# Performance work log

Measured on AMD Instinct MI355X. Metric: run time of the kernel, lower is better.

## Reference

```python
import jax, jax.numpy as jnp
import numpy as np

B, T, C = 256, 2048, 64
WINDOW_RATIO = 0.1
SCALES = (0.5, 2.0)
WARP_SIZE = int(np.ceil(WINDOW_RATIO * T))            # 205, matches np.ceil(...).astype(int)
L_MAX = (T - WARP_SIZE) + int(WARP_SIZE * max(SCALES))  # max warped length (scale=2.0) = 2253


def setup_inputs() -> dict:
    key = jax.random.key(0)
    k1, k2, k3 = jax.random.split(key, 3)
    x = jax.random.normal(k1, (B, T, C), dtype=jnp.float32)
    # np.random.choice(scales, B)
    warp_scales = jnp.asarray(SCALES, jnp.float32)[jax.random.randint(k2, (B,), 0, len(SCALES))]
    # np.random.randint(low=1, high=T - warp_size - 1, size=B)
    window_starts = jax.random.randint(k3, (B,), 1, T - WARP_SIZE - 1).astype(jnp.int32)
    return {"x": x, "warp_scales": warp_scales, "window_starts": window_starts}


def _lerp_gather(arr, pos, max_idx):
    # arr: [B, L, C]; pos: [B, N] fractional indices -> [B, N, C] linear interp
    p0 = jnp.floor(pos)
    frac = (pos - p0)[..., None]
    i0 = p0.astype(jnp.int32)
    i1 = jnp.minimum(i0 + 1, max_idx)
    g0 = jnp.take_along_axis(arr, i0[..., None], axis=1)
    g1 = jnp.take_along_axis(arr, i1[..., None], axis=1)
    return g0 * (1.0 - frac) + g1 * frac


def _window_warp(x, warp_scales, window_starts):
    Bx, Tx, Cx = x.shape
    # int(warp_size * scale): truncation == floor for positive values
    new_len = jnp.floor(WARP_SIZE * warp_scales)          # [B] float, resampled window length
    L = (Tx - WARP_SIZE) + new_len                        # [B] float, total warped length per sample
    start = window_starts.astype(x.dtype)[:, None]        # [B,1]
    nl = new_len[:, None]                                 # [B,1]

    # Stage 1: build warped sequence of padded length L_MAX via fractional gather from x.
    # warped[j] = x[j]                       for j < start
    #           = interp(x window) at s_win  for start <= j < start+new_len
    #           = x[j - new_len + warp_size] for j >= start+new_len (garbage past L, never read)
    j = jnp.arange(L_MAX, dtype=x.dtype)[None, :]         # [1, L_MAX]
    in_win = (j >= start) & (j < start + nl)
    after = j >= start + nl
    s_win = start + (j - start) * (WARP_SIZE - 1) / jnp.maximum(nl - 1.0, 1.0)
    s = jnp.where(in_win, s_win, jnp.where(after, j - nl + WARP_SIZE, j))
    s = jnp.clip(s, 0.0, Tx - 1)
    warped = _lerp_gather(x, s, Tx - 1)                   # [B, L_MAX, C]

    # Stage 2: np.interp(arange(T), linspace(0, T-1, L), warped) == linear interp of
    # warped at fractional index u = t * (L-1) / (T-1)
    t = jnp.arange(Tx, dtype=x.dtype)[None, :]            # [1, T]
    u = t * (L[:, None] - 1.0) / (Tx - 1.0)
    u = jnp.clip(u, 0.0, L[:, None] - 1.0)
    return _lerp_gather(warped, u, L_MAX - 1)             # [B, T, C]


def reference(x, warp_scales, window_starts):
    return _window_warp(x, warp_scales, window_starts)
```

## Files before the change

kernel.cpp:

```cpp
#include <hip/hip_runtime.h>

constexpr int Bn     = 256;
constexpr int Tn     = 2048;
constexpr int Cn     = 64;
constexpr int WARPSZ = 205;
constexpr int LMAX   = 2253;

typedef float f32x4 __attribute__((ext_vector_type(4)));

__device__ __forceinline__ void map_j(float jf, float start, float nl, float rdenom,
                                      int& i0, int& i1, float& fr) {
    bool in_win = (jf >= start) && (jf < start + nl);
    bool after  = (jf >= start + nl);
    float s_win   = start + (jf - start) * rdenom;
    float s_after = jf - nl + (float)WARPSZ;
    float s = in_win ? s_win : (after ? s_after : jf);
    s = fminf(fmaxf(s, 0.0f), (float)(Tn - 1));
    float p0 = floorf(s);
    fr = s - p0;
    i0 = (int)p0;
    i1 = min(i0 + 1, Tn - 1);
}

__global__ __launch_bounds__(256) void window_warp_kernel(
        const float* __restrict__ x,
        const float* __restrict__ scales,
        const int*   __restrict__ starts,
        float*       __restrict__ out) {
    int b     = blockIdx.x >> 6;
    int tbase = ((blockIdx.x & 63) << 5) | (threadIdx.x >> 4);
    int cg    = threadIdx.x & 15;

    float scale = scales[b];
    float start = (float)starts[b];
    float nl    = floorf((float)WARPSZ * scale);
    float Lm1   = (float)(Tn - WARPSZ) + nl - 1.0f;
    float rdenom = (float)(WARPSZ - 1) / fmaxf(nl - 1.0f, 1.0f);

    const f32x4* __restrict__ xb   = (const f32x4*)(x   + (size_t)b * (Tn * Cn));
    f32x4*       __restrict__ outb = (f32x4*)      (out + (size_t)b * (Tn * Cn));

    int   i00[2], i01[2], i10[2], i11[2];
    float f0[2], f1[2], fu[2];

    #pragma unroll
    for (int k = 0; k < 2; ++k) {
        int t = tbase + 16 * k;
        float u = ((float)t * Lm1) / (float)(Tn - 1);
        u = fminf(fmaxf(u, 0.0f), Lm1);
        float q0 = floorf(u);
        fu[k] = u - q0;
        int j0 = (int)q0;
        int j1 = min(j0 + 1, LMAX - 1);
        map_j((float)j0, start, nl, rdenom, i00[k], i01[k], f0[k]);
        map_j((float)j1, start, nl, rdenom, i10[k], i11[k], f1[k]);
    }

    f32x4 A0[2], A1[2], B0[2], B1[2];
    #pragma unroll
    for (int k = 0; k < 2; ++k) {
        A0[k] = xb[i00[k] * 16 + cg];
        A1[k] = xb[i01[k] * 16 + cg];
        B0[k] = xb[i10[k] * 16 + cg];
        B1[k] = xb[i11[k] * 16 + cg];
    }

    #pragma unroll
    for (int k = 0; k < 2; ++k) {
        int t = tbase + 16 * k;
        float g0 = 1.0f - f0[k], g1 = 1.0f - f1[k], gu = 1.0f - fu[k];
        f32x4 v0 = A0[k] * g0 + A1[k] * f0[k];
        f32x4 v1 = B0[k] * g1 + B1[k] * f1[k];
        f32x4 r  = v0 * gu + v1 * fu[k];
        __builtin_nontemporal_store(r, &outb[t * 16 + cg]);
    }
}

extern "C" void kernel_launch(void* const* d_in, const int* in_sizes, int n_in,
                              void* d_out, int out_size, void* d_ws, size_t ws_size,
                              hipStream_t stream) {
    const float* x      = (const float*)d_in[0];
    const float* scales = (const float*)d_in[1];
    const int*   starts = (const int*)d_in[2];
    float* out = (float*)d_out;

    int total_threads = Bn * Tn * (Cn / 4) / 2;
    int blocks = total_threads / 256;
    window_warp_kernel<<<blocks, 256, 0, stream>>>(x, scales, starts, out);
}
```

Measured before the change: 228.1 us.

## Stage per-block input rows in LDS via async global_load_lds and remap block order

```diff
diff --git a/kernel.cpp b/kernel.cpp
--- a/kernel.cpp
+++ b/kernel.cpp
@@ -1,10 +1,14 @@
 #include <hip/hip_runtime.h>
+#include <stdint.h>
 
 constexpr int Bn     = 256;
 constexpr int Tn     = 2048;
 constexpr int Cn     = 64;
 constexpr int WARPSZ = 205;
 constexpr int LMAX   = 2253;
+
+constexpr int TB = 32;
+constexpr int NR = 72;
 
 typedef float f32x4 __attribute__((ext_vector_type(4)));
 
@@ -27,8 +31,13 @@
         const float* __restrict__ scales,
         const int*   __restrict__ starts,
         float*       __restrict__ out) {
-    int b     = blockIdx.x >> 6;
-    int tbase = ((blockIdx.x & 63) << 5) | (threadIdx.x >> 4);
+    __shared__ f32x4 smem[NR * (Cn / 4)];
+
+    int n    = blockIdx.x;
+    int bidx = ((n & 7) << 11) | (n >> 3);
+    int b     = bidx >> 6;
+    int t0    = (bidx & 63) << 5;
+    int tslot = threadIdx.x >> 4;
     int cg    = threadIdx.x & 15;
 
     float scale = scales[b];
@@ -37,15 +46,33 @@
     float Lm1   = (float)(Tn - WARPSZ) + nl - 1.0f;
     float rdenom = (float)(WARPSZ - 1) / fmaxf(nl - 1.0f, 1.0f);
 
-    const f32x4* __restrict__ xb   = (const f32x4*)(x   + (size_t)b * (Tn * Cn));
-    f32x4*       __restrict__ outb = (f32x4*)      (out + (size_t)b * (Tn * Cn));
+    float u0 = ((float)t0 * Lm1) / (float)(Tn - 1);
+    u0 = fminf(fmaxf(u0, 0.0f), Lm1);
+    int j00 = (int)floorf(u0);
+    int r0a, r0b; float fr0;
+    map_j((float)j00, start, nl, rdenom, r0a, r0b, fr0);
+    int rbase = min(r0a, Tn - NR);
+
+    {
+        const float* gbase = x + (size_t)b * (Tn * Cn) + rbase * Cn;
+        int wave = threadIdx.x >> 6;
+        int lane = threadIdx.x & 63;
+        float* sm = (float*)smem;
+        #pragma unroll
+        for (int c = wave; c < (NR * Cn * 4) / 1024; c += 4) {
+            __builtin_amdgcn_global_load_lds(
+                (const __attribute__((address_space(1))) uint32_t*)(gbase + c * 256 + lane * 4),
+                (__attribute__((address_space(3))) uint32_t*)(sm + c * 256),
+                16, 0, 0);
+        }
+    }
+    __syncthreads();
 
     int   i00[2], i01[2], i10[2], i11[2];
     float f0[2], f1[2], fu[2];
-
     #pragma unroll
     for (int k = 0; k < 2; ++k) {
-        int t = tbase + 16 * k;
+        int t = t0 + tslot + 16 * k;
         float u = ((float)t * Lm1) / (float)(Tn - 1);
         u = fminf(fmaxf(u, 0.0f), Lm1);
         float q0 = floorf(u);
@@ -59,15 +86,16 @@
     f32x4 A0[2], A1[2], B0[2], B1[2];
     #pragma unroll
     for (int k = 0; k < 2; ++k) {
-        A0[k] = xb[i00[k] * 16 + cg];
-        A1[k] = xb[i01[k] * 16 + cg];
-        B0[k] = xb[i10[k] * 16 + cg];
-        B1[k] = xb[i11[k] * 16 + cg];
+        A0[k] = smem[(i00[k] - rbase) * 16 + cg];
+        A1[k] = smem[(i01[k] - rbase) * 16 + cg];
+        B0[k] = smem[(i10[k] - rbase) * 16 + cg];
+        B1[k] = smem[(i11[k] - rbase) * 16 + cg];
     }
 
+    f32x4* outb = (f32x4*)(out + (size_t)b * (Tn * Cn));
     #pragma unroll
     for (int k = 0; k < 2; ++k) {
-        int t = tbase + 16 * k;
+        int t = t0 + tslot + 16 * k;
         float g0 = 1.0f - f0[k], g1 = 1.0f - f1[k], gu = 1.0f - fu[k];
         f32x4 v0 = A0[k] * g0 + A1[k] * f0[k];
         f32x4 v1 = B0[k] * g1 + B1[k] * f1[k];
@@ -84,7 +112,6 @@
     const int*   starts = (const int*)d_in[2];
     float* out = (float*)d_out;
 
-    int total_threads = Bn * Tn * (Cn / 4) / 2;
-    int blocks = total_threads / 256;
+    int blocks = Bn * Tn / TB;
     window_warp_kernel<<<blocks, 256, 0, stream>>>(x, scales, starts, out);
 }
```

After: 237.5 us. +4.1%, slower.
